# Optimization experiments

Hardware: AMD Instinct MI355X
Metric: run time of the kernel (lower is better)

The kernel has to match this reference:

```python
import jax, jax.numpy as jnp
import numpy as np

# Static module config (matches init_kwargs; note forward requires P == Np)
Np = 60   # particles
P  = 60   # per-particle features
Nv = 14   # secondary vertices
S  = 5    # per-vertex features
De = 20
Do = 24
HID = 60
NPP = Np * (Np - 1)
NPV = Np * Nv

# Edge list replacing the dense one-hot Rr/Rs matmuls.
# Edges are all ordered pairs (i, j), i != j, ordered by receiver i then sender j,
# so edges with the same receiver are contiguous (enables reshape+sum scatter).
_pairs = np.array([(i, j) for i in range(Np) for j in range(Np) if i != j], dtype=np.int64)
RECV = jnp.asarray(_pairs[:, 0])  # [NPP]
SEND = jnp.asarray(_pairs[:, 1])  # [NPP]


def _mlp(h, W1, b1, W2, b2):
    return jax.nn.relu(h @ W1 + b1) @ W2 + b2


def setup_inputs() -> dict:
    key = jax.random.key(0)
    ks = jax.random.split(key, 9)
    B = 1024

    def lin(k, fi, fo):
        kw, kb = jax.random.split(k)
        s = 1.0 / np.sqrt(fi)
        W = jax.random.uniform(kw, (fi, fo), minval=-s, maxval=s, dtype=jnp.float32)
        b = jax.random.uniform(kb, (fo,), minval=-s, maxval=s, dtype=jnp.float32)
        return W, b

    W1_pp, b1_pp = lin(ks[0], 2 * P, HID)
    W2_pp, b2_pp = lin(ks[1], HID, De)
    W1_pv, b1_pv = lin(ks[2], P + S, HID)
    W2_pv, b2_pv = lin(ks[3], HID, De)
    W1_o, b1_o = lin(ks[4], P + De, HID)
    W2_o, b2_o = lin(ks[5], HID, Do)
    Wc, bc = lin(ks[6], Do, 1)
    x = jax.random.normal(ks[7], (B, P, Np), dtype=jnp.float32)
    y = jax.random.normal(ks[8], (B, S, Nv), dtype=jnp.float32)
    return dict(x=x, y=y,
                W1_pp=W1_pp, b1_pp=b1_pp, W2_pp=W2_pp, b2_pp=b2_pp,
                W1_pv=W1_pv, b1_pv=b1_pv, W2_pv=W2_pv, b2_pv=b2_pv,
                W1_o=W1_o, b1_o=b1_o, W2_o=W2_o, b2_o=b2_o,
                Wc=Wc, bc=bc)


def reference(x, y, W1_pp, b1_pp, W2_pp, b2_pp, W1_pv, b1_pv, W2_pv, b2_pv,
              W1_o, b1_o, W2_o, b2_o, Wc, bc):
    Bb = x.shape[0]
    # particle-particle branch: gather (x @ Rr, x @ Rs) as index takes
    Orr = jnp.take(x, RECV, axis=2)                  # [B, P, NPP]
    Ors = jnp.take(x, SEND, axis=2)                  # [B, P, NPP]
    Bcat = jnp.concatenate([Orr, Ors], axis=1)       # [B, 2P, NPP]
    # Faithful to the original: B.view(-1, 2P) WITHOUT transposing (row-major flatten)
    E = _mlp(Bcat.reshape(-1, 2 * P), W1_pp, b1_pp, W2_pp, b2_pp).reshape(Bb, NPP, De)
    E = jnp.swapaxes(E, 1, 2)                        # [B, De, NPP]
    # scatter-sum E @ Rr.T : edges grouped by receiver -> reshape+sum
    Ebar_pp = E.reshape(Bb, De, Np, Np - 1).sum(axis=-1)   # [B, De, Np]
    # particle-vertex branch: t = i*Nv + v
    Ork = jnp.repeat(x, Nv, axis=2)                  # [B, P, NPV]  (x @ Rk)
    Orv = jnp.tile(y, (1, 1, Np))                    # [B, S, NPV]  (y @ Rv)
    C = jnp.swapaxes(jnp.concatenate([Ork, Orv], axis=1), 1, 2)  # [B, NPV, P+S]
    F = _mlp(C.reshape(-1, P + S), W1_pv, b1_pv, W2_pv, b2_pv).reshape(Bb, NPV, De)
    F = jnp.swapaxes(F, 1, 2)                        # [B, De, NPV]
    Ebar_pv = F.reshape(Bb, De, Np, Nv).sum(axis=-1)  # F @ Rk.T  -> [B, De, Np]
    Ebar = jnp.swapaxes(Ebar_pp + Ebar_pv, 1, 2)     # [B, Np, De]
    J = jnp.concatenate([x, Ebar], axis=2)           # [B, Np, P+De] (requires P==Np)
    O = _mlp(J.reshape(-1, P + De), W1_o, b1_o, W2_o, b2_o).reshape(Bb, Np, Do)
    O = O.sum(axis=1)                                # transpose+sum over particles -> [B, Do]
    O = O @ Wc + bc                                  # [B, 1]
    return jax.nn.sigmoid(O)
```

## Files before the change

### kernel.cpp

```cpp
#include <hip/hip_runtime.h>
#include <hip/hip_bf16.h>
#include <math.h>

typedef __attribute__((ext_vector_type(8))) short short8;
typedef __attribute__((ext_vector_type(4))) float f32x4;

namespace {
constexpr int XB0    = 0;
constexpr int YB0    = 7440;
constexpr int ZSB    = 7580;
constexpr int EBF_B  = 7584;
constexpr int WLDS_B = 12384;
constexpr int EBB_B  = 24672;
constexpr int HLDS_B = 28768;
constexpr int OSUM_B = 37984;
constexpr int SM_BYTES = 38080;

constexpr int NTAB_PP = 222 * 4 * 64 * 8;
constexpr int NTAB_PV = 53 * 3 * 64 * 8;
constexpr int NTAB_O  = 4 * 3 * 64 * 8;
constexpr int TABPP_B = 0;
constexpr int TABPV_B = TABPP_B + NTAB_PP * 2;
constexpr int TABO_B  = TABPV_B + NTAB_PV * 2;
constexpr int WPP1_B  = TABO_B + NTAB_O * 2;
constexpr int WPP2_B  = WPP1_B + 16 * 1024;
constexpr int WPV1_B  = WPP2_B + 4 * 1024;
constexpr int WPV2_B  = WPV1_B + 12 * 1024;
constexpr int WO1_B   = WPV2_B + 4 * 1024;
constexpr int WO2_B   = WO1_B + 12 * 1024;
constexpr int BIAS_B  = WO2_B + 4 * 1024;
}

__device__ __forceinline__ short f2bfs(float f) {
  __hip_bfloat16 h = __float2bfloat16(f);
  short s;
  __builtin_memcpy(&s, &h, 2);
  return s;
}

__global__ __launch_bounds__(256) void build_tables(char* wsb) {
  int t = blockIdx.x * 256 + threadIdx.x;
  unsigned short* tpp = (unsigned short*)(wsb + TABPP_B);
  unsigned short* tpv = (unsigned short*)(wsb + TABPV_B);
  unsigned short* tou = (unsigned short*)(wsb + TABO_B);
  if (t < NTAB_PP) {
    int j = t & 7, l = (t >> 3) & 63, blk = t >> 9;
    int ks = blk & 3, mt = blk >> 2;
    int rr = mt * 16 + (l & 15), k = ks * 32 + (l >> 4) * 8 + j;
    unsigned off = ZSB;
    if (rr < 3540 && k < 120) {
      unsigned p = (unsigned)rr * 120u + (unsigned)k;
      unsigned f = p / 3540u, e = p - f * 3540u;
      unsigned i = e / 59u, jj = e - i * 59u;
      unsigned col = (f < 60u) ? i : ((jj < i) ? jj : jj + 1u);
      unsigned ft = (f < 60u) ? f : f - 60u;
      off = XB0 + (ft * 62u + col) * 2u;
    }
    tpp[t] = (unsigned short)off;
    return;
  }
  t -= NTAB_PP;
  if (t < NTAB_PV) {
    int j = t & 7, l = (t >> 3) & 63, blk = t >> 9;
    int ks = blk % 3, mt = blk / 3;
    int tt = mt * 16 + (l & 15), k = ks * 32 + (l >> 4) * 8 + j;
    unsigned off = ZSB;
    if (tt < 840 && k < 65) {
      int i = tt / 14, v = tt - i * 14;
      off = (k < 60) ? (unsigned)(XB0 + (k * 62 + i) * 2)
                     : (unsigned)(YB0 + ((k - 60) * 14 + v) * 2);
    }
    tpv[t] = (unsigned short)off;
    return;
  }
  t -= NTAB_PV;
  if (t < NTAB_O) {
    int j = t & 7, l = (t >> 3) & 63, blk = t >> 9;
    int ks = blk % 3, mt = blk / 3;
    int r = mt * 16 + (l & 15), k = ks * 32 + (l >> 4) * 8 + j;
    unsigned off = ZSB;
    if (r < 60 && k < 80)
      off = (k < 60) ? (unsigned)(XB0 + (r * 62 + k) * 2)
                     : (unsigned)(EBB_B + (r * 20 + (k - 60)) * 2);
    tou[t] = (unsigned short)off;
  }
}

__global__ __launch_bounds__(256) void build_wfrag(char* wsb,
    const float* W1pp, const float* W2pp, const float* W1pv, const float* W2pv,
    const float* W1o, const float* W2o,
    const float* b1pp, const float* b2pp, const float* b1pv, const float* b2pv,
    const float* b1o, const float* b2o) {
  int t = blockIdx.x * 256 + threadIdx.x;
  if (t < 13312) {
    const float* W; int Kt, Nt, NTt; unsigned* dst; int local;
    if (t < 4096)       { W = W1pp; Kt = 120; Nt = 60; NTt = 4; dst = (unsigned*)(wsb + WPP1_B); local = t; }
    else if (t < 5120)  { W = W2pp; Kt = 60;  Nt = 20; NTt = 2; dst = (unsigned*)(wsb + WPP2_B); local = t - 4096; }
    else if (t < 8192)  { W = W1pv; Kt = 65;  Nt = 60; NTt = 4; dst = (unsigned*)(wsb + WPV1_B); local = t - 5120; }
    else if (t < 9216)  { W = W2pv; Kt = 60;  Nt = 20; NTt = 2; dst = (unsigned*)(wsb + WPV2_B); local = t - 8192; }
    else if (t < 12288) { W = W1o;  Kt = 80;  Nt = 60; NTt = 4; dst = (unsigned*)(wsb + WO1_B);  local = t - 9216; }
    else                { W = W2o;  Kt = 60;  Nt = 24; NTt = 2; dst = (unsigned*)(wsb + WO2_B);  local = t - 12288; }
    int d = local & 3, l = (local >> 2) & 63, rest = local >> 8;
    int nt = rest % NTt, ks = rest / NTt;
    int k = ks * 32 + (l >> 4) * 8 + 2 * d, n = nt * 16 + (l & 15);
    float v0 = (k < Kt && n < Nt) ? W[k * Nt + n] : 0.f;
    float v1 = (k + 1 < Kt && n < Nt) ? W[(k + 1) * Nt + n] : 0.f;
    unsigned u0 = (unsigned short)f2bfs(v0);
    unsigned u1 = (unsigned short)f2bfs(v1);
    dst[local] = u0 | (u1 << 16);
    return;
  }
  t -= 13312;
  if (t < 288) {
    float* bd = (float*)(wsb + BIAS_B);
    float v = 0.f;
    if (t < 64)       { if (t < 60) v = b1pp[t]; }
    else if (t < 96)  { int n = t - 64;  if (n < 20) v = b2pp[n]; }
    else if (t < 160) { int n = t - 96;  if (n < 60) v = b1pv[n]; }
    else if (t < 192) { int n = t - 160; if (n < 20) v = b2pv[n]; }
    else if (t < 256) { int n = t - 192; if (n < 60) v = b1o[n]; }
    else              { int n = t - 256; if (n < 24) v = b2o[n]; }
    bd[t] = v;
  }
}

template <int NKS>
__device__ __forceinline__ void mlp_core(
    const uint4 (&tw)[NKS], int lane,
    const short8* wf1,
    const short8 (&wf2r)[4],
    const float (&b1v)[4], const float (&b2v)[2],
    const unsigned char* smb, short (*hrow)[72], f32x4 (&a2)[2])
{
  const int cl = lane & 15, qq = lane >> 4;

  f32x4 acc[4];
#pragma unroll
  for (int nt = 0; nt < 4; ++nt) {
    float bv = b1v[nt];
    acc[nt] = (f32x4){bv, bv, bv, bv};
  }

#pragma unroll
  for (int ks = 0; ks < NKS; ++ks) {
    short8 af;
    af[0] = *(const short*)(smb + (tw[ks].x & 0xffffu));
    af[1] = *(const short*)(smb + (tw[ks].x >> 16));
    af[2] = *(const short*)(smb + (tw[ks].y & 0xffffu));
    af[3] = *(const short*)(smb + (tw[ks].y >> 16));
    af[4] = *(const short*)(smb + (tw[ks].z & 0xffffu));
    af[5] = *(const short*)(smb + (tw[ks].z >> 16));
    af[6] = *(const short*)(smb + (tw[ks].w & 0xffffu));
    af[7] = *(const short*)(smb + (tw[ks].w >> 16));
#pragma unroll
    for (int nt = 0; nt < 4; ++nt) {
      short8 wf = wf1[(ks * 4 + nt) * 64 + lane];
      acc[nt] = __builtin_amdgcn_mfma_f32_16x16x32_bf16(af, wf, acc[nt], 0, 0, 0);
    }
  }

#pragma unroll
  for (int nt = 0; nt < 4; ++nt)
#pragma unroll
    for (int r = 0; r < 4; ++r)
      hrow[qq * 4 + r][nt * 16 + cl] = f2bfs(fmaxf(acc[nt][r], 0.f));

#pragma unroll
  for (int nt = 0; nt < 2; ++nt) {
    float bv = b2v[nt];
    a2[nt] = (f32x4){bv, bv, bv, bv};
  }
#pragma unroll
  for (int k2 = 0; k2 < 2; ++k2) {
    short8 h = *(const short8*)&hrow[cl][k2 * 32 + qq * 8];
#pragma unroll
    for (int nt = 0; nt < 2; ++nt)
      a2[nt] = __builtin_amdgcn_mfma_f32_16x16x32_bf16(h, wf2r[k2 * 2 + nt], a2[nt], 0, 0, 0);
  }
}

template <int DIV, int LIM>
__device__ __forceinline__ void scatter_e(const f32x4 (&a2)[2], int rb, float* eb, int cl) {
  int riA = rb / DIV, riB = (rb + 3) / DIV;
#pragma unroll
  for (int nt = 0; nt < 2; ++nt) {
    int col = nt * 16 + cl;
    if (col < 20) {
      if (riA == riB && rb + 3 < LIM) {
        atomicAdd(&eb[riA * 20 + col], a2[nt][0] + a2[nt][1] + a2[nt][2] + a2[nt][3]);
      } else {
#pragma unroll
        for (int r = 0; r < 4; ++r) {
          int rr = rb + r;
          if (rr < LIM) atomicAdd(&eb[(rr / DIV) * 20 + col], a2[nt][r]);
        }
      }
    }
  }
}

__global__ __launch_bounds__(256, 4) void fused_kernel(
    const float* __restrict__ x, const float* __restrict__ y,
    const float* __restrict__ Wc, const float* __restrict__ Bc,
    const char* __restrict__ wsb, float* __restrict__ out) {
  __shared__ __align__(16) unsigned char SM[SM_BYTES];

  const int b = blockIdx.x;
  const int tid = threadIdx.x;
  const int w = tid >> 6;
  const int lane = tid & 63;
  const int cl = lane & 15, q4 = (lane >> 4) * 4;

  float* ebf = (float*)(SM + EBF_B);
  float* osum = (float*)(SM + OSUM_B);
  short (*hrow)[72] = (short(*)[72])(SM + HLDS_B + w * 2304);
  const float* biasf = (const float*)(wsb + BIAS_B);

  {
    short* xb = (short*)(SM + XB0);
    for (int k = tid; k < 3600; k += 256) {
      int r = k / 60, c = k - r * 60;
      xb[r * 62 + c] = f2bfs(x[(size_t)b * 3600 + k]);
    }
    short* yb = (short*)(SM + YB0);
    if (tid < 70) yb[tid] = f2bfs(y[(size_t)b * 70 + tid]);
    if (tid == 0) *(short*)(SM + ZSB) = 0;
    for (int k = tid; k < 1200; k += 256) ebf[k] = 0.f;
    if (tid < 24) osum[tid] = 0.f;
    uint4* d = (uint4*)(SM + WLDS_B);
    const uint4* s = (const uint4*)(wsb + WPP1_B);
    for (int k = tid; k < 1024; k += 256) d[k] = s[k];
  }
  __syncthreads();

  {
    const short8* wf1 = (const short8*)(SM + WLDS_B);
    const uint4* tab = (const uint4*)(wsb + TABPP_B);
    short8 wf2r[4];
#pragma unroll
    for (int i = 0; i < 4; ++i) wf2r[i] = ((const short8*)(wsb + WPP2_B))[i * 64 + lane];
    float b1v[4], b2v[2];
#pragma unroll
    for (int nt = 0; nt < 4; ++nt) b1v[nt] = biasf[0 + nt * 16 + cl];
#pragma unroll
    for (int nt = 0; nt < 2; ++nt) b2v[nt] = biasf[64 + nt * 16 + cl];

    uint4 twn[4];
#pragma unroll
    for (int ks = 0; ks < 4; ++ks) twn[ks] = tab[(w * 4 + ks) * 64 + lane];
    for (int mt = w; mt < 222; mt += 4) {
      uint4 twc[4];
#pragma unroll
      for (int ks = 0; ks < 4; ++ks) twc[ks] = twn[ks];
      int mtn = mt + 4;
      if (mtn < 222) {
#pragma unroll
        for (int ks = 0; ks < 4; ++ks) twn[ks] = tab[(mtn * 4 + ks) * 64 + lane];
      }
      f32x4 a2[2];
      mlp_core<4>(twc, lane, wf1, wf2r, b1v, b2v, SM, hrow, a2);
      scatter_e<59, 3540>(a2, mt * 16 + q4, ebf, cl);
    }
  }

  __syncthreads();
  {
    uint4* d = (uint4*)(SM + WLDS_B);
    const uint4* s = (const uint4*)(wsb + WPV1_B);
    for (int k = tid; k < 768; k += 256) d[k] = s[k];
  }
  __syncthreads();

  {
    const short8* wf1 = (const short8*)(SM + WLDS_B);
    const uint4* tab = (const uint4*)(wsb + TABPV_B);
    short8 wf2r[4];
#pragma unroll
    for (int i = 0; i < 4; ++i) wf2r[i] = ((const short8*)(wsb + WPV2_B))[i * 64 + lane];
    float b1v[4], b2v[2];
#pragma unroll
    for (int nt = 0; nt < 4; ++nt) b1v[nt] = biasf[96 + nt * 16 + cl];
#pragma unroll
    for (int nt = 0; nt < 2; ++nt) b2v[nt] = biasf[160 + nt * 16 + cl];

    uint4 twn[3];
    if (w < 53) {
#pragma unroll
      for (int ks = 0; ks < 3; ++ks) twn[ks] = tab[(w * 3 + ks) * 64 + lane];
    }
    for (int mt = w; mt < 53; mt += 4) {
      uint4 twc[3];
#pragma unroll
      for (int ks = 0; ks < 3; ++ks) twc[ks] = twn[ks];
      int mtn = mt + 4;
      if (mtn < 53) {
#pragma unroll
        for (int ks = 0; ks < 3; ++ks) twn[ks] = tab[(mtn * 3 + ks) * 64 + lane];
      }
      f32x4 a2[2];
      mlp_core<3>(twc, lane, wf1, wf2r, b1v, b2v, SM, hrow, a2);
      scatter_e<14, 840>(a2, mt * 16 + q4, ebf, cl);
    }
  }

  __syncthreads();
  {
    short* ebb = (short*)(SM + EBB_B);
    for (int k = tid; k < 1200; k += 256) ebb[k] = f2bfs(ebf[k]);
    uint4* d = (uint4*)(SM + WLDS_B);
    const uint4* s = (const uint4*)(wsb + WO1_B);
    for (int k = tid; k < 768; k += 256) d[k] = s[k];
  }
  __syncthreads();

  {
    const short8* wf1 = (const short8*)(SM + WLDS_B);
    const uint4* tab = (const uint4*)(wsb + TABO_B);
    short8 wf2r[4];
#pragma unroll
    for (int i = 0; i < 4; ++i) wf2r[i] = ((const short8*)(wsb + WO2_B))[i * 64 + lane];
    float b1v[4], b2v[2];
#pragma unroll
    for (int nt = 0; nt < 4; ++nt) b1v[nt] = biasf[192 + nt * 16 + cl];
#pragma unroll
    for (int nt = 0; nt < 2; ++nt) b2v[nt] = biasf[256 + nt * 16 + cl];

    uint4 twc[3];
#pragma unroll
    for (int ks = 0; ks < 3; ++ks) twc[ks] = tab[(w * 3 + ks) * 64 + lane];
    f32x4 a2[2];
    mlp_core<3>(twc, lane, wf1, wf2r, b1v, b2v, SM, hrow, a2);

    int rb = w * 16 + q4;
#pragma unroll
    for (int nt = 0; nt < 2; ++nt) {
      int col = nt * 16 + cl;
      if (col < 24) {
        if (rb + 3 < 60) {
          atomicAdd(&osum[col], a2[nt][0] + a2[nt][1] + a2[nt][2] + a2[nt][3]);
        } else {
#pragma unroll
          for (int r = 0; r < 4; ++r)
            if (rb + r < 60) atomicAdd(&osum[col], a2[nt][r]);
        }
      }
    }
  }

  __syncthreads();
  if (tid == 0) {
    float sd = Bc[0];
#pragma unroll
    for (int o = 0; o < 24; ++o) sd = fmaf(osum[o], Wc[o], sd);
    out[b] = 1.f / (1.f + expf(-sd));
  }
}

extern "C" void kernel_launch(void* const* d_in, const int* in_sizes, int n_in,
                              void* d_out, int out_size, void* d_ws, size_t ws_size,
                              hipStream_t stream) {
  const float* x     = (const float*)d_in[0];
  const float* y     = (const float*)d_in[1];
  const float* W1_pp = (const float*)d_in[2];
  const float* b1_pp = (const float*)d_in[3];
  const float* W2_pp = (const float*)d_in[4];
  const float* b2_pp = (const float*)d_in[5];
  const float* W1_pv = (const float*)d_in[6];
  const float* b1_pv = (const float*)d_in[7];
  const float* W2_pv = (const float*)d_in[8];
  const float* b2_pv = (const float*)d_in[9];
  const float* W1_o  = (const float*)d_in[10];
  const float* b1_o  = (const float*)d_in[11];
  const float* W2_o  = (const float*)d_in[12];
  const float* b2_o  = (const float*)d_in[13];
  const float* Wc    = (const float*)d_in[14];
  const float* bc    = (const float*)d_in[15];
  float* out = (float*)d_out;
  char* wsb = (char*)d_ws;

  const int Bb = in_sizes[0] / 3600;
  const int tab_total = NTAB_PP + NTAB_PV + NTAB_O;

  build_tables<<<(tab_total + 255) / 256, 256, 0, stream>>>(wsb);
  build_wfrag<<<(13312 + 288 + 255) / 256, 256, 0, stream>>>(wsb,
      W1_pp, W2_pp, W1_pv, W2_pv, W1_o, W2_o,
      b1_pp, b2_pp, b1_pv, b2_pv, b1_o, b2_o);
  fused_kernel<<<Bb, 256, 0, stream>>>(x, y, Wc, bc, wsb, out);
}
```

Measured before the change: 353.9 us.

## Pin first-layer weight fragments in registers and drop LDS weight staging

Each wave now loads the layer-1 and layer-2 weight fragments straight from global memory into registers and pins them there, so the LDS weight buffer, its copy loops and the extra barriers are gone. Per-tile LDS reads of weights are removed and LDS use shrinks. The hidden-activation store is rewritten as one vectorized 4-short write per row, with the layer-2 weight K index permuted to match the new column order. Launch bounds drop from 4 to 3 waves per SIMD to allow the higher register count, which reduces occupancy.

```diff
diff --git a/kernel.cpp b/kernel.cpp
--- a/kernel.cpp
+++ b/kernel.cpp
@@ -3,18 +3,19 @@
 #include <math.h>
 
 typedef __attribute__((ext_vector_type(8))) short short8;
+typedef __attribute__((ext_vector_type(4))) short short4v;
 typedef __attribute__((ext_vector_type(4))) float f32x4;
+typedef __attribute__((ext_vector_type(4))) unsigned int u32x4;
 
 namespace {
 constexpr int XB0    = 0;
 constexpr int YB0    = 7440;
 constexpr int ZSB    = 7580;
 constexpr int EBF_B  = 7584;
-constexpr int WLDS_B = 12384;
-constexpr int EBB_B  = 24672;
-constexpr int HLDS_B = 28768;
-constexpr int OSUM_B = 37984;
-constexpr int SM_BYTES = 38080;
+constexpr int EBB_B  = 12384;
+constexpr int HLDS_B = 14784;
+constexpr int OSUM_B = 24000;
+constexpr int SM_BYTES = 24096;
 
 constexpr int NTAB_PP = 222 * 4 * 64 * 8;
 constexpr int NTAB_PV = 53 * 3 * 64 * 8;
@@ -35,6 +36,12 @@
   __hip_bfloat16 h = __float2bfloat16(f);
   short s;
   __builtin_memcpy(&s, &h, 2);
+  return s;
+}
+
+__device__ __forceinline__ short8 as_s8(u32x4 v) {
+  short8 s;
+  __builtin_memcpy(&s, &v, 16);
   return s;
 }
 
@@ -93,18 +100,23 @@
     const float* b1o, const float* b2o) {
   int t = blockIdx.x * 256 + threadIdx.x;
   if (t < 13312) {
-    const float* W; int Kt, Nt, NTt; unsigned* dst; int local;
-    if (t < 4096)       { W = W1pp; Kt = 120; Nt = 60; NTt = 4; dst = (unsigned*)(wsb + WPP1_B); local = t; }
-    else if (t < 5120)  { W = W2pp; Kt = 60;  Nt = 20; NTt = 2; dst = (unsigned*)(wsb + WPP2_B); local = t - 4096; }
-    else if (t < 8192)  { W = W1pv; Kt = 65;  Nt = 60; NTt = 4; dst = (unsigned*)(wsb + WPV1_B); local = t - 5120; }
-    else if (t < 9216)  { W = W2pv; Kt = 60;  Nt = 20; NTt = 2; dst = (unsigned*)(wsb + WPV2_B); local = t - 8192; }
-    else if (t < 12288) { W = W1o;  Kt = 80;  Nt = 60; NTt = 4; dst = (unsigned*)(wsb + WO1_B);  local = t - 9216; }
-    else                { W = W2o;  Kt = 60;  Nt = 24; NTt = 2; dst = (unsigned*)(wsb + WO2_B);  local = t - 12288; }
+    const float* W; int Kt, Nt, NTt; unsigned* dst; int local; bool st2;
+    if (t < 4096)       { W = W1pp; Kt = 120; Nt = 60; NTt = 4; dst = (unsigned*)(wsb + WPP1_B); local = t; st2 = false; }
+    else if (t < 5120)  { W = W2pp; Kt = 60;  Nt = 20; NTt = 2; dst = (unsigned*)(wsb + WPP2_B); local = t - 4096; st2 = true; }
+    else if (t < 8192)  { W = W1pv; Kt = 65;  Nt = 60; NTt = 4; dst = (unsigned*)(wsb + WPV1_B); local = t - 5120; st2 = false; }
+    else if (t < 9216)  { W = W2pv; Kt = 60;  Nt = 20; NTt = 2; dst = (unsigned*)(wsb + WPV2_B); local = t - 8192; st2 = true; }
+    else if (t < 12288) { W = W1o;  Kt = 80;  Nt = 60; NTt = 4; dst = (unsigned*)(wsb + WO1_B);  local = t - 9216; st2 = false; }
+    else                { W = W2o;  Kt = 60;  Nt = 24; NTt = 2; dst = (unsigned*)(wsb + WO2_B);  local = t - 12288; st2 = true; }
     int d = local & 3, l = (local >> 2) & 63, rest = local >> 8;
     int nt = rest % NTt, ks = rest / NTt;
-    int k = ks * 32 + (l >> 4) * 8 + 2 * d, n = nt * 16 + (l & 15);
-    float v0 = (k < Kt && n < Nt) ? W[k * Nt + n] : 0.f;
-    float v1 = (k + 1 < Kt && n < Nt) ? W[(k + 1) * Nt + n] : 0.f;
+    int k0 = ks * 32 + (l >> 4) * 8 + 2 * d, k1 = k0 + 1;
+    if (st2) {
+      k0 = (k0 & 3) * 16 + (k0 >> 2);
+      k1 = (k1 & 3) * 16 + (k1 >> 2);
+    }
+    int n = nt * 16 + (l & 15);
+    float v0 = (k0 < Kt && n < Nt) ? W[k0 * Nt + n] : 0.f;
+    float v1 = (k1 < Kt && n < Nt) ? W[k1 * Nt + n] : 0.f;
     unsigned u0 = (unsigned short)f2bfs(v0);
     unsigned u1 = (unsigned short)f2bfs(v1);
     dst[local] = u0 | (u1 << 16);
@@ -127,8 +139,7 @@
 template <int NKS>
 __device__ __forceinline__ void mlp_core(
     const uint4 (&tw)[NKS], int lane,
-    const short8* wf1,
-    const short8 (&wf2r)[4],
+    const u32x4 (&wf1r)[NKS * 4], const u32x4 (&wf2r)[4],
     const float (&b1v)[4], const float (&b2v)[2],
     const unsigned char* smb, short (*hrow)[72], f32x4 (&a2)[2])
 {
@@ -153,17 +164,19 @@
     af[6] = *(const short*)(smb + (tw[ks].w & 0xffffu));
     af[7] = *(const short*)(smb + (tw[ks].w >> 16));
 #pragma unroll
-    for (int nt = 0; nt < 4; ++nt) {
-      short8 wf = wf1[(ks * 4 + nt) * 64 + lane];
-      acc[nt] = __builtin_amdgcn_mfma_f32_16x16x32_bf16(af, wf, acc[nt], 0, 0, 0);
-    }
-  }
-
-#pragma unroll
-  for (int nt = 0; nt < 4; ++nt)
-#pragma unroll
-    for (int r = 0; r < 4; ++r)
-      hrow[qq * 4 + r][nt * 16 + cl] = f2bfs(fmaxf(acc[nt][r], 0.f));
+    for (int nt = 0; nt < 4; ++nt)
+      acc[nt] = __builtin_amdgcn_mfma_f32_16x16x32_bf16(af, as_s8(wf1r[ks * 4 + nt]), acc[nt], 0, 0, 0);
+  }
+
+#pragma unroll
+  for (int r = 0; r < 4; ++r) {
+    short4v hw;
+    hw[0] = f2bfs(fmaxf(acc[0][r], 0.f));
+    hw[1] = f2bfs(fmaxf(acc[1][r], 0.f));
+    hw[2] = f2bfs(fmaxf(acc[2][r], 0.f));
+    hw[3] = f2bfs(fmaxf(acc[3][r], 0.f));
+    *(short4v*)&hrow[qq * 4 + r][cl * 4] = hw;
+  }
 
 #pragma unroll
   for (int nt = 0; nt < 2; ++nt) {
@@ -175,7 +188,7 @@
     short8 h = *(const short8*)&hrow[cl][k2 * 32 + qq * 8];
 #pragma unroll
     for (int nt = 0; nt < 2; ++nt)
-      a2[nt] = __builtin_amdgcn_mfma_f32_16x16x32_bf16(h, wf2r[k2 * 2 + nt], a2[nt], 0, 0, 0);
+      a2[nt] = __builtin_amdgcn_mfma_f32_16x16x32_bf16(h, as_s8(wf2r[k2 * 2 + nt]), a2[nt], 0, 0, 0);
   }
 }
 
@@ -199,7 +212,15 @@
   }
 }
 
-__global__ __launch_bounds__(256, 4) void fused_kernel(
+template <int NF>
+__device__ __forceinline__ void load_pin(u32x4 (&r)[NF], const char* src, int lane) {
+#pragma unroll
+  for (int i = 0; i < NF; ++i) r[i] = ((const u32x4*)src)[i * 64 + lane];
+#pragma unroll
+  for (int i = 0; i < NF; ++i) asm volatile("" : "+v"(r[i]));
+}
+
+__global__ __launch_bounds__(256, 3) void fused_kernel(
     const float* __restrict__ x, const float* __restrict__ y,
     const float* __restrict__ Wc, const float* __restrict__ Bc,
     const char* __restrict__ wsb, float* __restrict__ out) {
@@ -227,18 +248,14 @@
     if (tid == 0) *(short*)(SM + ZSB) = 0;
     for (int k = tid; k < 1200; k += 256) ebf[k] = 0.f;
     if (tid < 24) osum[tid] = 0.f;
-    uint4* d = (uint4*)(SM + WLDS_B);
-    const uint4* s = (const uint4*)(wsb + WPP1_B);
-    for (int k = tid; k < 1024; k += 256) d[k] = s[k];
-  }
-  __syncthreads();
-
-  {
-    const short8* wf1 = (const short8*)(SM + WLDS_B);
+  }
+  __syncthreads();
+
+  {
     const uint4* tab = (const uint4*)(wsb + TABPP_B);
-    short8 wf2r[4];
-#pragma unroll
-    for (int i = 0; i < 4; ++i) wf2r[i] = ((const short8*)(wsb + WPP2_B))[i * 64 + lane];
+    u32x4 wf1r[16], wf2r[4];
+    load_pin<16>(wf1r, wsb + WPP1_B, lane);
+    load_pin<4>(wf2r, wsb + WPP2_B, lane);
     float b1v[4], b2v[2];
 #pragma unroll
     for (int nt = 0; nt < 4; ++nt) b1v[nt] = biasf[0 + nt * 16 + cl];
@@ -258,25 +275,18 @@
         for (int ks = 0; ks < 4; ++ks) twn[ks] = tab[(mtn * 4 + ks) * 64 + lane];
       }
       f32x4 a2[2];
-      mlp_core<4>(twc, lane, wf1, wf2r, b1v, b2v, SM, hrow, a2);
+      mlp_core<4>(twc, lane, wf1r, wf2r, b1v, b2v, SM, hrow, a2);
       scatter_e<59, 3540>(a2, mt * 16 + q4, ebf, cl);
     }
   }
 
   __syncthreads();
-  {
-    uint4* d = (uint4*)(SM + WLDS_B);
-    const uint4* s = (const uint4*)(wsb + WPV1_B);
-    for (int k = tid; k < 768; k += 256) d[k] = s[k];
-  }
-  __syncthreads();
-
-  {
-    const short8* wf1 = (const short8*)(SM + WLDS_B);
+
+  {
     const uint4* tab = (const uint4*)(wsb + TABPV_B);
-    short8 wf2r[4];
-#pragma unroll
-    for (int i = 0; i < 4; ++i) wf2r[i] = ((const short8*)(wsb + WPV2_B))[i * 64 + lane];
+    u32x4 wf1r[12], wf2r[4];
+    load_pin<12>(wf1r, wsb + WPV1_B, lane);
+    load_pin<4>(wf2r, wsb + WPV2_B, lane);
     float b1v[4], b2v[2];
 #pragma unroll
     for (int nt = 0; nt < 4; ++nt) b1v[nt] = biasf[96 + nt * 16 + cl];
@@ -284,10 +294,8 @@
     for (int nt = 0; nt < 2; ++nt) b2v[nt] = biasf[160 + nt * 16 + cl];
 
     uint4 twn[3];
-    if (w < 53) {
-#pragma unroll
-      for (int ks = 0; ks < 3; ++ks) twn[ks] = tab[(w * 3 + ks) * 64 + lane];
-    }
+#pragma unroll
+    for (int ks = 0; ks < 3; ++ks) twn[ks] = tab[(w * 3 + ks) * 64 + lane];
     for (int mt = w; mt < 53; mt += 4) {
       uint4 twc[3];
 #pragma unroll
@@ -298,7 +306,7 @@
         for (int ks = 0; ks < 3; ++ks) twn[ks] = tab[(mtn * 3 + ks) * 64 + lane];
       }
       f32x4 a2[2];
-      mlp_core<3>(twc, lane, wf1, wf2r, b1v, b2v, SM, hrow, a2);
+      mlp_core<3>(twc, lane, wf1r, wf2r, b1v, b2v, SM, hrow, a2);
       scatter_e<14, 840>(a2, mt * 16 + q4, ebf, cl);
     }
   }
@@ -307,18 +315,14 @@
   {
     short* ebb = (short*)(SM + EBB_B);
     for (int k = tid; k < 1200; k += 256) ebb[k] = f2bfs(ebf[k]);
-    uint4* d = (uint4*)(SM + WLDS_B);
-    const uint4* s = (const uint4*)(wsb + WO1_B);
-    for (int k = tid; k < 768; k += 256) d[k] = s[k];
-  }
-  __syncthreads();
-
-  {
-    const short8* wf1 = (const short8*)(SM + WLDS_B);
+  }
+  __syncthreads();
+
+  {
     const uint4* tab = (const uint4*)(wsb + TABO_B);
-    short8 wf2r[4];
-#pragma unroll
-    for (int i = 0; i < 4; ++i) wf2r[i] = ((const short8*)(wsb + WO2_B))[i * 64 + lane];
+    u32x4 wf1r[12], wf2r[4];
+    load_pin<12>(wf1r, wsb + WO1_B, lane);
+    load_pin<4>(wf2r, wsb + WO2_B, lane);
     float b1v[4], b2v[2];
 #pragma unroll
     for (int nt = 0; nt < 4; ++nt) b1v[nt] = biasf[192 + nt * 16 + cl];
@@ -329,7 +333,7 @@
 #pragma unroll
     for (int ks = 0; ks < 3; ++ks) twc[ks] = tab[(w * 3 + ks) * 64 + lane];
     f32x4 a2[2];
-    mlp_core<3>(twc, lane, wf1, wf2r, b1v, b2v, SM, hrow, a2);
+    mlp_core<3>(twc, lane, wf1r, wf2r, b1v, b2v, SM, hrow, a2);
 
     int rb = w * 16 + q4;
 #pragma unroll
```

Measured after the change: 314.7 us. 1.12x faster.
